# Performance work log

Hardware: AMD Instinct MI355X
Metric: run time of the kernel (lower is better)

Reference implementation:

```python
import jax, jax.numpy as jnp
import numpy as np

C = 1024        # BIGNET_DIM
GS = 128        # group_size
R = 4           # lora_dim
NL = 12         # 4 blocks x 3 QLoRALinear
N = 4096        # batch
NG = C * C // GS  # 8192 groups per layer
EPS = 1e-5


def dequant4(q4, norm):
    # q4: [NG, GS//2] int32 in [0,255] (two nibbles per byte), norm: [NG,1] f32
    low = q4 & 0xF
    high = (q4 >> 4) & 0xF
    # interleave: even positions = low nibble, odd = high nibble
    q8 = jnp.stack([low, high], axis=-1).reshape(q4.shape[0], GS)
    w = (q8.astype(jnp.float32) / 15.0 * 2.0 - 1.0) * norm
    return w.reshape(C, C)  # [out_features, in_features]


def qlora_linear(x, q4, norm, a, b):
    # base 4-bit dequant matmul + low-rank LoRA add (bias=False)
    w = dequant4(q4, norm)
    return x @ w.T + (x @ a.T) @ b.T  # [N,C]


def block(x, q4s, norms, As, Bs):
    h = qlora_linear(x, q4s[0], norms[0], As[0], Bs[0])
    h = jax.nn.relu(h)
    h = qlora_linear(h, q4s[1], norms[1], As[1], Bs[1])
    h = jax.nn.relu(h)
    h = qlora_linear(h, q4s[2], norms[2], As[2], Bs[2])
    return h + x  # residual


def layer_norm(x, g, b):
    mu = jnp.mean(x, axis=-1, keepdims=True)
    var = jnp.var(x, axis=-1, keepdims=True)
    return (x - mu) * jax.lax.rsqrt(var + EPS) * g + b


def setup_inputs() -> dict:
    key = jax.random.key(0)
    ks = jax.random.split(key, 5)
    x = jax.random.normal(ks[0], (N, C), dtype=jnp.float32)
    w_q4 = jax.random.randint(ks[1], (NL, NG, GS // 2), 0, 256, dtype=jnp.int32)
    w_norm = jax.random.uniform(ks[2], (NL, NG, 1), dtype=jnp.float32, minval=0.01, maxval=0.1)
    lora_a = jax.random.normal(ks[3], (NL, R, C), dtype=jnp.float32) * 0.02
    lora_b = jax.random.normal(ks[4], (NL, C, R), dtype=jnp.float32) * 0.02
    ln_g = jnp.ones((2, C), dtype=jnp.float32)
    ln_b = jnp.zeros((2, C), dtype=jnp.float32)
    return {"x": x, "w_q4": w_q4, "w_norm": w_norm, "lora_a": lora_a,
            "lora_b": lora_b, "ln_g": ln_g, "ln_b": ln_b}


def reference(x, w_q4, w_norm, lora_a, lora_b, ln_g, ln_b):
    h = block(x, w_q4[0:3], w_norm[0:3], lora_a[0:3], lora_b[0:3])
    h = layer_norm(h, ln_g[0], ln_b[0])
    h = block(h, w_q4[3:6], w_norm[3:6], lora_a[3:6], lora_b[3:6])
    h = block(h, w_q4[6:9], w_norm[6:9], lora_a[6:9], lora_b[6:9])
    h = layer_norm(h, ln_g[1], ln_b[1])
    h = block(h, w_q4[9:12], w_norm[9:12], lora_a[9:12], lora_b[9:12])
    return h
```

## Files before the change

kernel.cpp:

```cpp
#include <hip/hip_runtime.h>

#define CD 1024
#define NB 4096

typedef __attribute__((ext_vector_type(8))) short short8;
typedef __attribute__((ext_vector_type(4))) short short4v;
typedef __attribute__((ext_vector_type(4))) float f32x4;
typedef __attribute__((ext_vector_type(4))) int int4v;

typedef __attribute__((address_space(1))) const void gv_t;
typedef __attribute__((address_space(3))) void lv_t;
#define GLOAD16(g, l) __builtin_amdgcn_global_load_lds((gv_t*)(g), (lv_t*)(l), 16, 0, 0)

__device__ __forceinline__ short f2bf(float f) {
  unsigned u = __float_as_uint(f);
  u = (u + 0x7FFFu + ((u >> 16) & 1u)) >> 16;
  return (short)u;
}
__device__ __forceinline__ float bf2f(short s) {
  return __uint_as_float(((unsigned)(unsigned short)s) << 16);
}

__global__ __launch_bounds__(256) void prep_kernel(const float* __restrict__ x,
                                                   short* __restrict__ xb,
                                                   const int* __restrict__ q4,
                                                   const float* __restrict__ nrm,
                                                   const float* __restrict__ la,
                                                   const float* __restrict__ lb,
                                                   short* __restrict__ Wb) {
  int bid = blockIdx.x;
  if (bid < 2048) {
    int i = (bid * 256 + threadIdx.x) * 8;
    f32x4 a = *(const f32x4*)(x + i);
    f32x4 b = *(const f32x4*)(x + i + 4);
    short8 o;
    o[0] = f2bf(a[0]); o[1] = f2bf(a[1]); o[2] = f2bf(a[2]); o[3] = f2bf(a[3]);
    o[4] = f2bf(b[0]); o[5] = f2bf(b[1]); o[6] = f2bf(b[2]); o[7] = f2bf(b[3]);
    *(short8*)(xb + i) = o;
    return;
  }
  int tidg = (bid - 2048) * 256 + threadIdx.x;
  int w0 = tidg * 4;
  int l = w0 >> 19;
  int wl = w0 & 524287;
  int g = wl >> 6;
  int j0 = wl & 63;
  int o = g >> 3;
  int kb = ((g & 7) << 7) + (j0 << 1);
  int4v q = *(const int4v*)(q4 + w0);
  float n = nrm[(l << 13) + g];
  float s = n * (2.0f / 15.0f);
  f32x4 B = *(const f32x4*)(lb + (((l << 10) + o) << 2));
  const float* A = la + (l << 12);
  float Ar[4][8];
#pragma unroll
  for (int r = 0; r < 4; ++r) {
    f32x4 u = *(const f32x4*)(A + r * CD + kb);
    f32x4 v = *(const f32x4*)(A + r * CD + kb + 4);
    Ar[r][0] = u[0]; Ar[r][1] = u[1]; Ar[r][2] = u[2]; Ar[r][3] = u[3];
    Ar[r][4] = v[0]; Ar[r][5] = v[1]; Ar[r][6] = v[2]; Ar[r][7] = v[3];
  }
  short8 outv;
#pragma unroll
  for (int p = 0; p < 8; ++p) {
    int qw = q[p >> 1];
    int nib = (qw >> ((p & 1) << 2)) & 15;
    float wv = (float)nib * s - n;
    wv += B[0] * Ar[0][p] + B[1] * Ar[1][p] + B[2] * Ar[2][p] + B[3] * Ar[3][p];
    outv[p] = f2bf(wv);
  }
  *(short8*)(Wb + (l << 20) + (o << 10) + kb) = outv;
}

template <int EPI>
__global__ __launch_bounds__(256, 2) void qgemm(const short* __restrict__ Act,
                                                const short* __restrict__ W,
                                                const short* __restrict__ Res,
                                                void* __restrict__ Out) {
  __shared__ __align__(16) short ldsA[2][128 * 64];
  __shared__ __align__(16) short ldsB[2][64 * 64];
  const int tid = threadIdx.x;
  const int lane = tid & 63;
  const int wid = tid >> 6;
  const int wr = wid >> 1, wc = wid & 1;
  const int m0 = blockIdx.x * 128;
  const int o0 = blockIdx.y * 64;

  const int srow = tid >> 3;
  const int gch = (tid & 7) ^ (srow & 7);
  const short* abase = Act + (long)(m0 + srow) * CD + (gch << 3);
  const short* bbase = W + (long)(o0 + srow) * CD + (gch << 3);

  auto stage = [&](int t, int buf) {
    const int koff = t << 6;
#pragma unroll
    for (int i = 0; i < 4; ++i)
      GLOAD16(abase + ((long)(i << 5)) * CD + koff, &ldsA[buf][(tid + (i << 8)) << 3]);
#pragma unroll
    for (int i = 0; i < 2; ++i)
      GLOAD16(bbase + ((long)(i << 5)) * CD + koff, &ldsB[buf][(tid + (i << 8)) << 3]);
  };

  f32x4 acc[4][2] = {};
  const int frow = lane & 15;
  const int fch = lane >> 4;
  const int fsw = lane & 7;

  stage(0, 0);
  for (int t = 0; t < 16; ++t) {
    __syncthreads();
    if (t < 15) stage(t + 1, (t + 1) & 1);
    const short* La = ldsA[t & 1];
    const short* Lb = ldsB[t & 1];
#pragma unroll
    for (int kk = 0; kk < 2; ++kk) {
      const int chb = (kk << 2) + fch;
      short8 af[4], wf[2];
#pragma unroll
      for (int m = 0; m < 4; ++m) {
        int row = (wr << 6) + (m << 4) + frow;
        af[m] = *(const short8*)(La + (row << 6) + ((chb ^ fsw) << 3));
      }
#pragma unroll
      for (int n = 0; n < 2; ++n) {
        int row = (wc << 5) + (n << 4) + frow;
        wf[n] = *(const short8*)(Lb + (row << 6) + ((chb ^ fsw) << 3));
      }
#pragma unroll
      for (int m = 0; m < 4; ++m)
#pragma unroll
        for (int n = 0; n < 2; ++n)
          acc[m][n] = __builtin_amdgcn_mfma_f32_16x16x32_bf16(wf[n], af[m], acc[m][n], 0, 0, 0);
    }
  }

  const int orow = m0 + (wr << 6) + frow;
  const int ocol = o0 + (wc << 5) + (fch << 2);
#pragma unroll
  for (int m = 0; m < 4; ++m) {
#pragma unroll
    for (int n = 0; n < 2; ++n) {
      long row = orow + (m << 4);
      int col = ocol + (n << 4);
      f32x4 v = acc[m][n];
      if (EPI == 0) {
        short4v ov;
        ov[0] = f2bf(fmaxf(v[0], 0.0f));
        ov[1] = f2bf(fmaxf(v[1], 0.0f));
        ov[2] = f2bf(fmaxf(v[2], 0.0f));
        ov[3] = f2bf(fmaxf(v[3], 0.0f));
        *(short4v*)((short*)Out + row * CD + col) = ov;
      } else if (EPI == 2) {
        short4v rv = *(const short4v*)(Res + row * CD + col);
        short4v ov;
        ov[0] = f2bf(v[0] + bf2f(rv[0]));
        ov[1] = f2bf(v[1] + bf2f(rv[1]));
        ov[2] = f2bf(v[2] + bf2f(rv[2]));
        ov[3] = f2bf(v[3] + bf2f(rv[3]));
        *(short4v*)((short*)Out + row * CD + col) = ov;
      } else {
        short4v rv = *(const short4v*)(Res + row * CD + col);
        f32x4 ov;
        ov[0] = v[0] + bf2f(rv[0]);
        ov[1] = v[1] + bf2f(rv[1]);
        ov[2] = v[2] + bf2f(rv[2]);
        ov[3] = v[3] + bf2f(rv[3]);
        *(f32x4*)((float*)Out + row * CD + col) = ov;
      }
    }
  }
}

__global__ __launch_bounds__(256) void ln_kernel(const short* __restrict__ in,
                                                 short* __restrict__ out,
                                                 const float* __restrict__ g,
                                                 const float* __restrict__ b) {
  __shared__ float rs_[4], rq_[4];
  int row = blockIdx.x, tid = threadIdx.x;
  int k = tid * 4;
  short4v v = *(const short4v*)(in + (long)row * CD + k);
  float f0 = bf2f(v[0]), f1 = bf2f(v[1]), f2 = bf2f(v[2]), f3 = bf2f(v[3]);
  float s = f0 + f1 + f2 + f3;
  float q = f0 * f0 + f1 * f1 + f2 * f2 + f3 * f3;
#pragma unroll
  for (int off = 1; off < 64; off <<= 1) {
    s += __shfl_xor(s, off);
    q += __shfl_xor(q, off);
  }
  if ((tid & 63) == 0) { rs_[tid >> 6] = s; rq_[tid >> 6] = q; }
  __syncthreads();
  s = rs_[0] + rs_[1] + rs_[2] + rs_[3];
  q = rq_[0] + rq_[1] + rq_[2] + rq_[3];
  float mu = s * (1.0f / 1024.0f);
  float var = q * (1.0f / 1024.0f) - mu * mu;
  float rstd = rsqrtf(var + 1e-5f);
  short4v o;
  o[0] = f2bf((f0 - mu) * rstd * g[k] + b[k]);
  o[1] = f2bf((f1 - mu) * rstd * g[k + 1] + b[k + 1]);
  o[2] = f2bf((f2 - mu) * rstd * g[k + 2] + b[k + 2]);
  o[3] = f2bf((f3 - mu) * rstd * g[k + 3] + b[k + 3]);
  *(short4v*)(out + (long)row * CD + k) = o;
}

extern "C" void kernel_launch(void* const* d_in, const int* in_sizes, int n_in,
                              void* d_out, int out_size, void* d_ws, size_t ws_size,
                              hipStream_t stream) {
  const float* x = (const float*)d_in[0];
  const int* q4 = (const int*)d_in[1];
  const float* nrm = (const float*)d_in[2];
  const float* la = (const float*)d_in[3];
  const float* lb = (const float*)d_in[4];
  const float* lng = (const float*)d_in[5];
  const float* lnb = (const float*)d_in[6];

  short* Wb = (short*)d_ws;
  short* buf0 = (short*)((char*)d_ws + (24u << 20));
  short* buf1 = buf0 + (long)NB * CD;
  short* buf2 = (short*)d_out;
  short* buf3 = buf2 + (long)NB * CD;
  float* outf = (float*)d_out;

  prep_kernel<<<dim3(8192), dim3(256), 0, stream>>>(x, buf0, q4, nrm, la, lb, Wb);

  dim3 gg(32, 16), bb(256);
  auto Wl = [&](int l) { return Wb + ((long)l << 20); };

  qgemm<0><<<gg, bb, 0, stream>>>(buf0, Wl(0), nullptr, buf1);
  qgemm<0><<<gg, bb, 0, stream>>>(buf1, Wl(1), nullptr, buf2);
  qgemm<2><<<gg, bb, 0, stream>>>(buf2, Wl(2), buf0, buf3);
  ln_kernel<<<dim3(4096), dim3(256), 0, stream>>>(buf3, buf0, lng, lnb);
  qgemm<0><<<gg, bb, 0, stream>>>(buf0, Wl(3), nullptr, buf1);
  qgemm<0><<<gg, bb, 0, stream>>>(buf1, Wl(4), nullptr, buf2);
  qgemm<2><<<gg, bb, 0, stream>>>(buf2, Wl(5), buf0, buf3);
  qgemm<0><<<gg, bb, 0, stream>>>(buf3, Wl(6), nullptr, buf1);
  qgemm<0><<<gg, bb, 0, stream>>>(buf1, Wl(7), nullptr, buf2);
  qgemm<2><<<gg, bb, 0, stream>>>(buf2, Wl(8), buf3, buf0);
  ln_kernel<<<dim3(4096), dim3(256), 0, stream>>>(buf0, buf1, lng + CD, lnb + CD);
  qgemm<0><<<gg, bb, 0, stream>>>(buf1, Wl(9), nullptr, buf2);
  qgemm<0><<<gg, bb, 0, stream>>>(buf2, Wl(10), nullptr, buf0);
  qgemm<3><<<gg, bb, 0, stream>>>(buf0, Wl(11), buf1, (void*)outf);
}
```

Baseline: 322.4 us.

## Use 128x128 tiles with 1024-thread blocks and XCD-aware block mapping

The GEMM tile grows from 128x64 with 4 waves to 128x128 with 16 waves, each wave computing a 32x32 sub-tile. The 2D grid becomes a 1D grid of 256 blocks, remapped so that blocks sharing an XCD cover neighbouring row tiles, for better L2 reuse. Each thread now issues one async global-to-LDS load per operand per stage. The risks are less MFMA work per LDS fragment read, costlier 16-wave barriers, and a launch bound of (1024,4) that may force a very tight register budget and cause spills.

```diff
diff --git a/kernel.cpp b/kernel.cpp
--- a/kernel.cpp
+++ b/kernel.cpp
@@ -73,35 +73,34 @@
 }
 
 template <int EPI>
-__global__ __launch_bounds__(256, 2) void qgemm(const short* __restrict__ Act,
-                                                const short* __restrict__ W,
-                                                const short* __restrict__ Res,
-                                                void* __restrict__ Out) {
+__global__ __launch_bounds__(1024, 4) void qgemm(const short* __restrict__ Act,
+                                                 const short* __restrict__ W,
+                                                 const short* __restrict__ Res,
+                                                 void* __restrict__ Out) {
   __shared__ __align__(16) short ldsA[2][128 * 64];
-  __shared__ __align__(16) short ldsB[2][64 * 64];
+  __shared__ __align__(16) short ldsB[2][128 * 64];
   const int tid = threadIdx.x;
   const int lane = tid & 63;
   const int wid = tid >> 6;
-  const int wr = wid >> 1, wc = wid & 1;
-  const int m0 = blockIdx.x * 128;
-  const int o0 = blockIdx.y * 64;
+  const int wr = wid >> 2;
+  const int wc = wid & 3;
+  const int f = blockIdx.x;
+  const int xcd = f & 7, c = f >> 3;
+  const int m0 = (((xcd << 2) | (c & 3)) << 7);
+  const int o0 = ((c >> 2) << 7);
 
   const int srow = tid >> 3;
-  const int gch = (tid & 7) ^ (srow & 7);
-  const short* abase = Act + (long)(m0 + srow) * CD + (gch << 3);
-  const short* bbase = W + (long)(o0 + srow) * CD + (gch << 3);
+  const int sch = (tid & 7) ^ (srow & 7);
+  const short* asrc = Act + (long)(m0 + srow) * CD + (sch << 3);
+  const short* bsrc = W + (long)(o0 + srow) * CD + (sch << 3);
 
   auto stage = [&](int t, int buf) {
     const int koff = t << 6;
-#pragma unroll
-    for (int i = 0; i < 4; ++i)
-      GLOAD16(abase + ((long)(i << 5)) * CD + koff, &ldsA[buf][(tid + (i << 8)) << 3]);
-#pragma unroll
-    for (int i = 0; i < 2; ++i)
-      GLOAD16(bbase + ((long)(i << 5)) * CD + koff, &ldsB[buf][(tid + (i << 8)) << 3]);
+    GLOAD16(asrc + koff, &ldsA[buf][tid << 3]);
+    GLOAD16(bsrc + koff, &ldsB[buf][tid << 3]);
   };
 
-  f32x4 acc[4][2] = {};
+  f32x4 acc[2][2] = {};
   const int frow = lane & 15;
   const int fch = lane >> 4;
   const int fsw = lane & 7;
@@ -114,30 +113,30 @@
     const short* Lb = ldsB[t & 1];
 #pragma unroll
     for (int kk = 0; kk < 2; ++kk) {
-      const int chb = (kk << 2) + fch;
-      short8 af[4], wf[2];
-#pragma unroll
-      for (int m = 0; m < 4; ++m) {
-        int row = (wr << 6) + (m << 4) + frow;
-        af[m] = *(const short8*)(La + (row << 6) + ((chb ^ fsw) << 3));
+      const int chsw = ((kk << 2) + fch) ^ fsw;
+      short8 af[2], wf[2];
+#pragma unroll
+      for (int m = 0; m < 2; ++m) {
+        int row = (wr << 5) + (m << 4) + frow;
+        af[m] = *(const short8*)(La + (row << 6) + (chsw << 3));
       }
 #pragma unroll
       for (int n = 0; n < 2; ++n) {
         int row = (wc << 5) + (n << 4) + frow;
-        wf[n] = *(const short8*)(Lb + (row << 6) + ((chb ^ fsw) << 3));
+        wf[n] = *(const short8*)(Lb + (row << 6) + (chsw << 3));
       }
 #pragma unroll
-      for (int m = 0; m < 4; ++m)
+      for (int m = 0; m < 2; ++m)
 #pragma unroll
         for (int n = 0; n < 2; ++n)
           acc[m][n] = __builtin_amdgcn_mfma_f32_16x16x32_bf16(wf[n], af[m], acc[m][n], 0, 0, 0);
     }
   }
 
-  const int orow = m0 + (wr << 6) + frow;
+  const int orow = m0 + (wr << 5) + frow;
   const int ocol = o0 + (wc << 5) + (fch << 2);
 #pragma unroll
-  for (int m = 0; m < 4; ++m) {
+  for (int m = 0; m < 2; ++m) {
 #pragma unroll
     for (int n = 0; n < 2; ++n) {
       long row = orow + (m << 4);
@@ -222,7 +221,7 @@
 
   prep_kernel<<<dim3(8192), dim3(256), 0, stream>>>(x, buf0, q4, nrm, la, lb, Wb);
 
-  dim3 gg(32, 16), bb(256);
+  dim3 gg(256), bb(1024);
   auto Wl = [&](int l) { return Wb + ((long)l << 20); };
 
   qgemm<0><<<gg, bb, 0, stream>>>(buf0, Wl(0), nullptr, buf1);
```

Result: faster. 306.8 us (-4.8%).
